# Kernel optimization log

Hardware: AMD Instinct MI355X
Metric: run time of the kernel (lower is better)

The kernel has to match this reference:

```python
import jax, jax.numpy as jnp
import numpy as np

SCALE = 1.0 / np.float32(64.0 ** 0.5)  # module hard-codes sqrt(64), not sqrt(d)


def setup_inputs() -> dict:
    key = jax.random.key(0)
    k1, k2 = jax.random.split(key)
    x = jax.random.normal(k1, (8, 2048, 1024), dtype=jnp.float32)
    kernel = jax.random.normal(k2, (3, 1024, 1024), dtype=jnp.float32) * 0.02
    return {"x": x, "kernel": kernel}


def reference(x, kernel):
    # x: [B, S, D], kernel: [3, D, O]
    wq = jnp.einsum('bsd,do->bso', x, kernel[0])
    wk = jnp.einsum('bsd,do->bso', x, kernel[1])
    wv = jnp.einsum('bsd,do->bso', x, kernel[2])
    scores = jnp.einsum('bqo,bko->bqk', wq, wk) * SCALE  # [B, S, S]
    attn = jax.nn.softmax(scores, axis=-1)
    return jnp.einsum('bqk,bko->bqo', attn, wv)  # [B, S, O]
```

## Files before the change

### kernel.cpp

```cpp
#include <hip/hip_runtime.h>

typedef _Float16 f16;
typedef f16 f16x8 __attribute__((ext_vector_type(8)));
typedef f16 f16x4 __attribute__((ext_vector_type(4)));
typedef float f32x4 __attribute__((ext_vector_type(4)));

#define GLD_LDS16(g, l) __builtin_amdgcn_global_load_lds( \
    (const __attribute__((address_space(1))) void*)(g),   \
    (__attribute__((address_space(3))) void*)(l), 16, 0, 0)

__device__ __forceinline__ void bar() {
    asm volatile("" ::: "memory");
    __builtin_amdgcn_s_barrier();
    asm volatile("" ::: "memory");
}
#define WAIT_VM(n) { asm volatile("s_waitcnt vmcnt(" #n ")" ::: "memory"); \
                     __builtin_amdgcn_sched_barrier(0); }
#define LGKM(n)    { asm volatile("s_waitcnt lgkmcnt(" #n ")" ::: "memory"); \
                     __builtin_amdgcn_sched_barrier(0); }

__global__ __launch_bounds__(256) void cast_f32_f16(const float* __restrict__ x,
                                                    f16* __restrict__ xh) {
    long i = ((long)blockIdx.x * 256 + threadIdx.x) * 8;
    float4 a = *(const float4*)&x[i];
    float4 b = *(const float4*)&x[i + 4];
    f16x8 v;
    v[0] = (f16)a.x; v[1] = (f16)a.y; v[2] = (f16)a.z; v[3] = (f16)a.w;
    v[4] = (f16)b.x; v[5] = (f16)b.y; v[6] = (f16)b.z; v[7] = (f16)b.w;
    *(f16x8*)&xh[i] = v;
}

__global__ __launch_bounds__(256) void cast_transpose_1k(const float* __restrict__ Wi,
                                                         f16* __restrict__ WTi) {
    __shared__ float tile[64][65];
    const int d0 = blockIdx.y * 64;
    const int o0 = blockIdx.x * 64;
    const int t = threadIdx.x;
#pragma unroll
    for (int j = 0; j < 4; ++j) {
        int idx = t + j * 256;
        int r = idx >> 4;
        int c4 = (idx & 15) * 4;
        float4 v = *(const float4*)&Wi[(long)(d0 + r) * 1024 + o0 + c4];
        tile[r][c4 + 0] = v.x; tile[r][c4 + 1] = v.y;
        tile[r][c4 + 2] = v.z; tile[r][c4 + 3] = v.w;
    }
    __syncthreads();
#pragma unroll
    for (int j = 0; j < 2; ++j) {
        int idx = t + j * 256;
        int ol = idx >> 3;
        int c8 = (idx & 7) * 8;
        f16x8 v;
#pragma unroll
        for (int e = 0; e < 8; ++e) v[e] = (f16)tile[c8 + e][ol];
        *(f16x8*)&WTi[(long)(o0 + ol) * 1024 + d0 + c8] = v;
    }
}

template <int MODE>
__global__ __launch_bounds__(512, 2)
void gemm256(const f16* __restrict__ A, const f16* __restrict__ B,
             void* __restrict__ Cv, const float* __restrict__ dinv,
             float* __restrict__ psum,
             int lda, int ldb, int K,
             long sA, long sB, long sC, int ldc, float scale) {
    extern __shared__ __align__(16) char smem[];
    const int tid = threadIdx.x;
    const int lane = tid & 63;
    const int wave = tid >> 6;
    const int wm = wave >> 2;
    const int wn = wave & 3;
    const int z = blockIdx.z;

    const int o_ = blockIdx.x + gridDim.x * blockIdx.y;
    const int nwg = gridDim.x * gridDim.y;
    const int sw = (o_ & 7) * (nwg >> 3) + (o_ >> 3);
    const int bx = sw % gridDim.x;
    const int by = sw / gridDim.x;

    const long m_base = (long)by * 256;
    const long n_base = (long)bx * 256;
    const f16* Ab = A + (long)z * sA;
    const f16* Bb = B + (long)z * sB;

    const int c_r0 = tid >> 3;
    const int c_col = ((tid & 7) * 8) ^ ((c_r0 & 7) << 3);
    const long oA0 = (m_base + c_r0) * (long)lda + c_col;
    const long oA1 = oA0 + 64L * lda;
    const long oB0 = (n_base + c_r0) * (long)ldb + c_col;
    const long oB1 = oB0 + 64L * ldb;

#define ST_A0(bf_, kt_) { long k0_ = (long)(kt_) * 64; \
    char* d_ = smem + (bf_) * 65536 + tid * 16; \
    GLD_LDS16(Ab + oA0 + k0_, d_); GLD_LDS16(Ab + oA1 + k0_, d_ + 8192); }
#define ST_A1(bf_, kt_) { long k0_ = (long)(kt_) * 64 + 128L * lda; \
    char* d_ = smem + (bf_) * 65536 + 16384 + tid * 16; \
    GLD_LDS16(Ab + oA0 + k0_, d_); GLD_LDS16(Ab + oA1 + k0_, d_ + 8192); }
#define ST_B0(bf_, kt_) { long k0_ = (long)(kt_) * 64; \
    char* d_ = smem + (bf_) * 65536 + 32768 + tid * 16; \
    GLD_LDS16(Bb + oB0 + k0_, d_); GLD_LDS16(Bb + oB1 + k0_, d_ + 8192); }
#define ST_B1(bf_, kt_) { long k0_ = (long)(kt_) * 64 + 128L * ldb; \
    char* d_ = smem + (bf_) * 65536 + 49152 + tid * 16; \
    GLD_LDS16(Bb + oB0 + k0_, d_); GLD_LDS16(Bb + oB1 + k0_, d_ + 8192); }

    const int fr = lane & 15;
    const int rq = lane >> 4;
    const int cs0 = (rq * 16) ^ ((lane & 7) << 4);
    const int cs1 = cs0 ^ 64;
    const int aoff = wm * 16384 + fr * 128;
    const int boff = 32768 + (wn >> 1) * 16384 + (wn & 1) * 8192 + fr * 128;

    f32x4 acc[8][4];
#pragma unroll
    for (int i = 0; i < 8; ++i)
#pragma unroll
        for (int j = 0; j < 4; ++j) acc[i][j] = (f32x4){0.f, 0.f, 0.f, 0.f};

    const int NT = K >> 6;

    ST_B0(0, 0); ST_B1(0, 0); ST_A0(0, 0); ST_A1(0, 0);
    WAIT_VM(4);
    ST_B0(1, 1); ST_B1(1, 1); ST_A0(1, 1);
    WAIT_VM(6);
    bar();

    for (int j = 0; j < NT; ++j) {
        char* bufb = smem + (j & 1) * 65536;
        const char* Ap = bufb + aoff;
        const char* Bp = bufb + boff;
        f16x8 af[4][2], bf[4][2];

#pragma unroll
        for (int i = 0; i < 4; ++i) {
            af[i][0] = *(const f16x8*)(Ap + i * 2048 + cs0);
            af[i][1] = *(const f16x8*)(Ap + i * 2048 + cs1);
        }
        __builtin_amdgcn_sched_barrier(0);
#pragma unroll
        for (int ni = 0; ni < 2; ++ni) {
            bf[ni][0] = *(const f16x8*)(Bp + ni * 2048 + cs0);
            bf[ni][1] = *(const f16x8*)(Bp + ni * 2048 + cs1);
        }
        __builtin_amdgcn_sched_barrier(0);
#pragma unroll
        for (int ni = 2; ni < 4; ++ni) {
            bf[ni][0] = *(const f16x8*)(Bp + ni * 2048 + cs0);
            bf[ni][1] = *(const f16x8*)(Bp + ni * 2048 + cs1);
        }
        if (j + 1 < NT) ST_A1((j + 1) & 1, j + 1);
        bar();
        LGKM(4);
        __builtin_amdgcn_s_setprio(1);
#pragma unroll
        for (int ks = 0; ks < 2; ++ks)
#pragma unroll
            for (int i = 0; i < 4; ++i)
#pragma unroll
                for (int n = 0; n < 2; ++n)
                    acc[i][n] = __builtin_amdgcn_mfma_f32_16x16x32_f16(
                        af[i][ks], bf[n][ks], acc[i][n], 0, 0, 0);
        __builtin_amdgcn_s_setprio(0);
        bar();

        LGKM(0);
        if (j + 2 < NT) ST_B0(j & 1, j + 2);
        bar();
        __builtin_amdgcn_s_setprio(1);
#pragma unroll
        for (int ks = 0; ks < 2; ++ks)
#pragma unroll
            for (int i = 0; i < 4; ++i)
#pragma unroll
                for (int n = 0; n < 2; ++n)
                    acc[i][2 + n] = __builtin_amdgcn_mfma_f32_16x16x32_f16(
                        af[i][ks], bf[2 + n][ks], acc[i][2 + n], 0, 0, 0);
        __builtin_amdgcn_s_setprio(0);
        bar();

#pragma unroll
        for (int i = 0; i < 4; ++i) {
            af[i][0] = *(const f16x8*)(Ap + (4 + i) * 2048 + cs0);
            af[i][1] = *(const f16x8*)(Ap + (4 + i) * 2048 + cs1);
        }
        if (j + 2 < NT) ST_B1(j & 1, j + 2);
        bar();
        LGKM(0);
        __builtin_amdgcn_s_setprio(1);
#pragma unroll
        for (int ks = 0; ks < 2; ++ks)
#pragma unroll
            for (int i = 0; i < 4; ++i)
#pragma unroll
                for (int n = 0; n < 2; ++n)
                    acc[4 + i][n] = __builtin_amdgcn_mfma_f32_16x16x32_f16(
                        af[i][ks], bf[n][ks], acc[4 + i][n], 0, 0, 0);
        __builtin_amdgcn_s_setprio(0);
        bar();

        if (j + 2 < NT) {
            ST_A0(j & 1, j + 2);
            WAIT_VM(6);
        } else if (j + 1 < NT) {
            WAIT_VM(0);
        }
        bar();
        __builtin_amdgcn_s_setprio(1);
#pragma unroll
        for (int ks = 0; ks < 2; ++ks)
#pragma unroll
            for (int i = 0; i < 4; ++i)
#pragma unroll
                for (int n = 0; n < 2; ++n)
                    acc[4 + i][2 + n] = __builtin_amdgcn_mfma_f32_16x16x32_f16(
                        af[i][ks], bf[2 + n][ks], acc[4 + i][2 + n], 0, 0, 0);
        __builtin_amdgcn_s_setprio(0);
        bar();
    }

    if constexpr (MODE == 0) {
        f16* C = (f16*)Cv + (long)z * sC;
        float p[8][4];
#pragma unroll
        for (int mi = 0; mi < 8; ++mi)
#pragma unroll
            for (int jj = 0; jj < 4; ++jj) p[mi][jj] = 0.f;
#pragma unroll
        for (int mi = 0; mi < 8; ++mi) {
            long r0 = m_base + wm * 128 + mi * 16 + rq * 4;
#pragma unroll
            for (int ni = 0; ni < 4; ++ni) {
                long c = n_base + wn * 64 + ni * 16 + fr;
#pragma unroll
                for (int jj = 0; jj < 4; ++jj) {
                    float e = __expf(acc[mi][ni][jj] * scale - 4.0f);
                    C[(r0 + jj) * (long)ldc + c] = (f16)e;
                    p[mi][jj] += e;
                }
            }
        }
#pragma unroll
        for (int mi = 0; mi < 8; ++mi)
#pragma unroll
            for (int jj = 0; jj < 4; ++jj)
#pragma unroll
                for (int o = 8; o; o >>= 1)
                    p[mi][jj] += __shfl_xor(p[mi][jj], o);
        float* wsum = (float*)smem;
        if (fr == 0) {
#pragma unroll
            for (int mi = 0; mi < 8; ++mi)
#pragma unroll
                for (int jj = 0; jj < 4; ++jj)
                    wsum[wn * 256 + wm * 128 + mi * 16 + rq * 4 + jj] = p[mi][jj];
        }
        bar();
        if (tid < 256) {
            float s = wsum[tid] + wsum[256 + tid] + wsum[512 + tid] + wsum[768 + tid];
            psum[((long)z * 2048 + m_base + tid) * 8 + bx] = s;
        }
    } else {
#pragma unroll
        for (int mi = 0; mi < 8; ++mi) {
            long r0 = m_base + wm * 128 + mi * 16 + rq * 4;
#pragma unroll
            for (int ni = 0; ni < 4; ++ni) {
                long c = n_base + wn * 64 + ni * 16 + fr;
                if constexpr (MODE == 1) {
                    f16* C = (f16*)Cv + (long)z * sC;
#pragma unroll
                    for (int jj = 0; jj < 4; ++jj)
                        C[(r0 + jj) * (long)ldc + c] = (f16)(acc[mi][ni][jj] * scale);
                } else if constexpr (MODE == 2) {
                    float* C = (float*)Cv + (long)z * sC;
#pragma unroll
                    for (int jj = 0; jj < 4; ++jj)
                        C[(r0 + jj) * (long)ldc + c] =
                            acc[mi][ni][jj] * dinv[(long)z * 2048 + r0 + jj];
                } else {
                    if (c < 1024) {
                        f16* T = (f16*)Cv;
#pragma unroll
                        for (int jj = 0; jj < 4; ++jj)
                            T[(r0 + jj) * 1024L + c] = (f16)acc[mi][ni][jj];
                    } else {
                        f16* VT = (f16*)((char*)Cv + 67108864);
                        long o = c - 1024;
                        long b = r0 >> 11;
                        long s = r0 & 2047;
                        f16x4 v;
#pragma unroll
                        for (int jj = 0; jj < 4; ++jj) v[jj] = (f16)acc[mi][ni][jj];
                        *(f16x4*)&VT[b * 2097152L + o * 2048L + s] = v;
                    }
                }
            }
        }
    }
#undef ST_A0
#undef ST_A1
#undef ST_B0
#undef ST_B1
}

__global__ __launch_bounds__(256) void reduce_dinv(const float* __restrict__ psum,
                                                   float* __restrict__ dinv) {
    int r = blockIdx.x * 256 + threadIdx.x;
    float4 a = *(const float4*)&psum[(long)r * 8];
    float4 b = *(const float4*)&psum[(long)r * 8 + 4];
    dinv[r] = 1.f / (a.x + a.y + a.z + a.w + b.x + b.y + b.z + b.w);
}

extern "C" void kernel_launch(void* const* d_in, const int* in_sizes, int n_in,
                              void* d_out, int out_size, void* d_ws, size_t ws_size,
                              hipStream_t stream) {
    const float* x = (const float*)d_in[0];
    const float* w = (const float*)d_in[1];
    float* out = (float*)d_out;
    char* ws = (char*)d_ws;

    f16* th  = (f16*)(ws + 0);
    f16* xh  = (f16*)(ws + 33554432);
    f16* vt  = (f16*)(ws + 67108864);
    char* spB = ws + 100663296;
    f16* whq = (f16*)(spB);
    f16* whk = (f16*)(spB + 2097152);
    f16* bTV = (f16*)(spB + 4194304);
    f16* sp  = (f16*)(spB);
    float* dinv = (float*)(ws + 0);
    float* psum = (float*)d_out;

    cast_f32_f16<<<1024, 256, 0, stream>>>(w, whq);
    cast_transpose_1k<<<dim3(16, 16), 256, 0, stream>>>(w + 2097152, bTV + 1048576);
    cast_f32_f16<<<8192, 256, 0, stream>>>(x, xh);

    gemm256<1><<<dim3(4, 4, 1), 512, 131072, stream>>>(
        whk, whq, bTV, nullptr, nullptr, 1024, 1024, 1024, 0L, 0L, 0L, 1024, 1.0f);

    gemm256<4><<<dim3(8, 64, 1), 512, 131072, stream>>>(
        xh, bTV, ws, nullptr, nullptr, 1024, 1024, 1024, 0L, 0L, 0L, 0, 1.0f);

    gemm256<0><<<dim3(8, 8, 8), 512, 131072, stream>>>(
        th, xh, sp, nullptr, psum, 1024, 1024, 1024,
        2097152L, 2097152L, 4194304L, 2048, 0.125f);

    reduce_dinv<<<64, 256, 0, stream>>>(psum, dinv);

    gemm256<2><<<dim3(4, 8, 8), 512, 131072, stream>>>(
        sp, vt, out, dinv, nullptr, 2048, 2048, 2048,
        4194304L, 2097152L, 2097152L, 1024, 1.0f);
}
```

Baseline: 295.6 us.

## Make GEMM workgroups loop over multiple N tiles and add small-tile weight GEMM

The main GEMM kernel gains a TILES parameter so each workgroup computes two consecutive 256-wide N tiles. It prefetches the next tile's first K stages while writing out the current epilogue, which halves the grid for the projection and score GEMMs. The tiny weight-product GEMM (whk·whqᵀ) moves to a new 128x128-tile kernel, gemm_mp, so it launches 64 workgroups instead of 16. The row-sum partials are now written per wave without an LDS reduction, so psum grows to 32 entries per row and reduce_dinv sums 32 values. The risk is fewer workgroups per launch (lower occupancy and worse tail balance) and more scattered psum writes.

```diff
diff --git a/kernel.cpp b/kernel.cpp
--- a/kernel.cpp
+++ b/kernel.cpp
@@ -58,7 +58,77 @@
     }
 }
 
-template <int MODE>
+__global__ __launch_bounds__(256, 2)
+void gemm_mp(const f16* __restrict__ A, const f16* __restrict__ B,
+             f16* __restrict__ C) {
+    __shared__ f16x8 ls[2][2][4][128];
+    const int tid = threadIdx.x;
+    const int lane = tid & 63;
+    const int wave = tid >> 6;
+    const int wm = wave >> 1;
+    const int wn = wave & 1;
+    const long m_base = (long)blockIdx.y * 128;
+    const long n_base = (long)blockIdx.x * 128;
+
+    const int i1 = tid + 256;
+    const int kb0 = tid >> 7, r0 = tid & 127;
+    const int kb1 = i1 >> 7, r1 = i1 & 127;
+    const f16* gA0 = A + (m_base + r0) * 1024L + kb0 * 8;
+    const f16* gA1 = A + (m_base + r1) * 1024L + kb1 * 8;
+    const f16* gB0 = B + (n_base + r0) * 1024L + kb0 * 8;
+    const f16* gB1 = B + (n_base + r1) * 1024L + kb1 * 8;
+
+    auto stage = [&](int buf, int k0) {
+        GLD_LDS16(gA0 + k0, &ls[buf][0][kb0][r0]);
+        GLD_LDS16(gA1 + k0, &ls[buf][0][kb1][r1]);
+        GLD_LDS16(gB0 + k0, &ls[buf][1][kb0][r0]);
+        GLD_LDS16(gB1 + k0, &ls[buf][1][kb1][r1]);
+    };
+
+    f32x4 acc[4][4];
+#pragma unroll
+    for (int i = 0; i < 4; ++i)
+#pragma unroll
+        for (int j = 0; j < 4; ++j) acc[i][j] = (f32x4){0.f, 0.f, 0.f, 0.f};
+
+    stage(0, 0);
+    WAIT_VM(0);
+    bar();
+    int cur = 0;
+    const int kb = lane >> 4;
+    const int fr = lane & 15;
+    for (int t = 0; t < 32; ++t) {
+        if (t + 1 < 32) stage(cur ^ 1, (t + 1) << 5);
+        f16x8 af[4], bf[4];
+#pragma unroll
+        for (int mi = 0; mi < 4; ++mi) af[mi] = ls[cur][0][kb][wm * 64 + mi * 16 + fr];
+#pragma unroll
+        for (int ni = 0; ni < 4; ++ni) bf[ni] = ls[cur][1][kb][wn * 64 + ni * 16 + fr];
+#pragma unroll
+        for (int mi = 0; mi < 4; ++mi)
+#pragma unroll
+            for (int ni = 0; ni < 4; ++ni)
+                acc[mi][ni] = __builtin_amdgcn_mfma_f32_16x16x32_f16(
+                    af[mi], bf[ni], acc[mi][ni], 0, 0, 0);
+        WAIT_VM(0);
+        bar();
+        cur ^= 1;
+    }
+    const int rq = lane >> 4;
+#pragma unroll
+    for (int mi = 0; mi < 4; ++mi) {
+        long r0_ = m_base + wm * 64 + mi * 16 + rq * 4;
+#pragma unroll
+        for (int ni = 0; ni < 4; ++ni) {
+            long c = n_base + wn * 64 + ni * 16 + fr;
+#pragma unroll
+            for (int j = 0; j < 4; ++j)
+                C[(r0_ + j) * 1024L + c] = (f16)acc[mi][ni][j];
+        }
+    }
+}
+
+template <int MODE, int TILES>
 __global__ __launch_bounds__(512, 2)
 void gemm256(const f16* __restrict__ A, const f16* __restrict__ B,
              void* __restrict__ Cv, const float* __restrict__ dinv,
@@ -76,11 +146,10 @@
     const int o_ = blockIdx.x + gridDim.x * blockIdx.y;
     const int nwg = gridDim.x * gridDim.y;
     const int sw = (o_ & 7) * (nwg >> 3) + (o_ >> 3);
-    const int bx = sw % gridDim.x;
+    const int bxb = sw % gridDim.x;
     const int by = sw / gridDim.x;
 
     const long m_base = (long)by * 256;
-    const long n_base = (long)bx * 256;
     const f16* Ab = A + (long)z * sA;
     const f16* Bb = B + (long)z * sB;
 
@@ -88,8 +157,8 @@
     const int c_col = ((tid & 7) * 8) ^ ((c_r0 & 7) << 3);
     const long oA0 = (m_base + c_r0) * (long)lda + c_col;
     const long oA1 = oA0 + 64L * lda;
-    const long oB0 = (n_base + c_r0) * (long)ldb + c_col;
-    const long oB1 = oB0 + 64L * ldb;
+    long oB0 = ((long)(bxb * TILES) * 256 + c_r0) * (long)ldb + c_col;
+    long oB1 = oB0 + 64L * ldb;
 
 #define ST_A0(bf_, kt_) { long k0_ = (long)(kt_) * 64; \
     char* d_ = smem + (bf_) * 65536 + tid * 16; \
@@ -111,12 +180,6 @@
     const int aoff = wm * 16384 + fr * 128;
     const int boff = 32768 + (wn >> 1) * 16384 + (wn & 1) * 8192 + fr * 128;
 
-    f32x4 acc[8][4];
-#pragma unroll
-    for (int i = 0; i < 8; ++i)
-#pragma unroll
-        for (int j = 0; j < 4; ++j) acc[i][j] = (f32x4){0.f, 0.f, 0.f, 0.f};
-
     const int NT = K >> 6;
 
     ST_B0(0, 0); ST_B1(0, 0); ST_A0(0, 0); ST_A1(0, 0);
@@ -125,176 +188,191 @@
     WAIT_VM(6);
     bar();
 
-    for (int j = 0; j < NT; ++j) {
-        char* bufb = smem + (j & 1) * 65536;
-        const char* Ap = bufb + aoff;
-        const char* Bp = bufb + boff;
-        f16x8 af[4][2], bf[4][2];
-
-#pragma unroll
-        for (int i = 0; i < 4; ++i) {
-            af[i][0] = *(const f16x8*)(Ap + i * 2048 + cs0);
-            af[i][1] = *(const f16x8*)(Ap + i * 2048 + cs1);
+    for (int tt = 0; tt < TILES; ++tt) {
+        const long n_base = (long)(bxb * TILES + tt) * 256;
+
+        f32x4 acc[8][4];
+#pragma unroll
+        for (int i = 0; i < 8; ++i)
+#pragma unroll
+            for (int j = 0; j < 4; ++j) acc[i][j] = (f32x4){0.f, 0.f, 0.f, 0.f};
+
+        for (int j = 0; j < NT; ++j) {
+            char* bufb = smem + (j & 1) * 65536;
+            const char* Ap = bufb + aoff;
+            const char* Bp = bufb + boff;
+            f16x8 af[4][2], bf[4][2];
+
+#pragma unroll
+            for (int i = 0; i < 4; ++i) {
+                af[i][0] = *(const f16x8*)(Ap + i * 2048 + cs0);
+                af[i][1] = *(const f16x8*)(Ap + i * 2048 + cs1);
+            }
+            __builtin_amdgcn_sched_barrier(0);
+#pragma unroll
+            for (int ni = 0; ni < 2; ++ni) {
+                bf[ni][0] = *(const f16x8*)(Bp + ni * 2048 + cs0);
+                bf[ni][1] = *(const f16x8*)(Bp + ni * 2048 + cs1);
+            }
+            __builtin_amdgcn_sched_barrier(0);
+#pragma unroll
+            for (int ni = 2; ni < 4; ++ni) {
+                bf[ni][0] = *(const f16x8*)(Bp + ni * 2048 + cs0);
+                bf[ni][1] = *(const f16x8*)(Bp + ni * 2048 + cs1);
+            }
+            if (j + 1 < NT) ST_A1((j + 1) & 1, j + 1);
+            bar();
+            LGKM(4);
+            __builtin_amdgcn_s_setprio(1);
+#pragma unroll
+            for (int ks = 0; ks < 2; ++ks)
+#pragma unroll
+                for (int i = 0; i < 4; ++i)
+#pragma unroll
+                    for (int n = 0; n < 2; ++n)
+                        acc[i][n] = __builtin_amdgcn_mfma_f32_16x16x32_f16(
+                            af[i][ks], bf[n][ks], acc[i][n], 0, 0, 0);
+            __builtin_amdgcn_s_setprio(0);
+            bar();
+
+            LGKM(0);
+            if (j + 2 < NT) ST_B0(j & 1, j + 2);
+            bar();
+            __builtin_amdgcn_s_setprio(1);
+#pragma unroll
+            for (int ks = 0; ks < 2; ++ks)
+#pragma unroll
+                for (int i = 0; i < 4; ++i)
+#pragma unroll
+                    for (int n = 0; n < 2; ++n)
+                        acc[i][2 + n] = __builtin_amdgcn_mfma_f32_16x16x32_f16(
+                            af[i][ks], bf[2 + n][ks], acc[i][2 + n], 0, 0, 0);
+            __builtin_amdgcn_s_setprio(0);
+            bar();
+
+#pragma unroll
+            for (int i = 0; i < 4; ++i) {
+                af[i][0] = *(const f16x8*)(Ap + (4 + i) * 2048 + cs0);
+                af[i][1] = *(const f16x8*)(Ap + (4 + i) * 2048 + cs1);
+            }
+            if (j + 2 < NT) ST_B1(j & 1, j + 2);
+            bar();
+            LGKM(0);
+            __builtin_amdgcn_s_setprio(1);
+#pragma unroll
+            for (int ks = 0; ks < 2; ++ks)
+#pragma unroll
+                for (int i = 0; i < 4; ++i)
+#pragma unroll
+                    for (int n = 0; n < 2; ++n)
+                        acc[4 + i][n] = __builtin_amdgcn_mfma_f32_16x16x32_f16(
+                            af[i][ks], bf[n][ks], acc[4 + i][n], 0, 0, 0);
+            __builtin_amdgcn_s_setprio(0);
+            bar();
+
+            if (j + 2 < NT) {
+                ST_A0(j & 1, j + 2);
+                WAIT_VM(6);
+            } else if (j + 1 < NT) {
+                WAIT_VM(0);
+            }
+            bar();
+            __builtin_amdgcn_s_setprio(1);
+#pragma unroll
+            for (int ks = 0; ks < 2; ++ks)
+#pragma unroll
+                for (int i = 0; i < 4; ++i)
+#pragma unroll
+                    for (int n = 0; n < 2; ++n)
+                        acc[4 + i][2 + n] = __builtin_amdgcn_mfma_f32_16x16x32_f16(
+                            af[i][ks], bf[2 + n][ks], acc[4 + i][2 + n], 0, 0, 0);
+            __builtin_amdgcn_s_setprio(0);
+            bar();
         }
-        __builtin_amdgcn_sched_barrier(0);
-#pragma unroll
-        for (int ni = 0; ni < 2; ++ni) {
-            bf[ni][0] = *(const f16x8*)(Bp + ni * 2048 + cs0);
-            bf[ni][1] = *(const f16x8*)(Bp + ni * 2048 + cs1);
+
+        if (tt + 1 < TILES) {
+            oB0 = ((long)(bxb * TILES + tt + 1) * 256 + c_r0) * (long)ldb + c_col;
+            oB1 = oB0 + 64L * ldb;
+            ST_B0(0, 0); ST_B1(0, 0); ST_A0(0, 0); ST_A1(0, 0);
+            ST_B0(1, 1); ST_B1(1, 1); ST_A0(1, 1);
         }
-        __builtin_amdgcn_sched_barrier(0);
-#pragma unroll
-        for (int ni = 2; ni < 4; ++ni) {
-            bf[ni][0] = *(const f16x8*)(Bp + ni * 2048 + cs0);
-            bf[ni][1] = *(const f16x8*)(Bp + ni * 2048 + cs1);
-        }
-        if (j + 1 < NT) ST_A1((j + 1) & 1, j + 1);
-        bar();
-        LGKM(4);
-        __builtin_amdgcn_s_setprio(1);
-#pragma unroll
-        for (int ks = 0; ks < 2; ++ks)
-#pragma unroll
-            for (int i = 0; i < 4; ++i)
-#pragma unroll
-                for (int n = 0; n < 2; ++n)
-                    acc[i][n] = __builtin_amdgcn_mfma_f32_16x16x32_f16(
-                        af[i][ks], bf[n][ks], acc[i][n], 0, 0, 0);
-        __builtin_amdgcn_s_setprio(0);
-        bar();
-
-        LGKM(0);
-        if (j + 2 < NT) ST_B0(j & 1, j + 2);
-        bar();
-        __builtin_amdgcn_s_setprio(1);
-#pragma unroll
-        for (int ks = 0; ks < 2; ++ks)
-#pragma unroll
-            for (int i = 0; i < 4; ++i)
-#pragma unroll
-                for (int n = 0; n < 2; ++n)
-                    acc[i][2 + n] = __builtin_amdgcn_mfma_f32_16x16x32_f16(
-                        af[i][ks], bf[2 + n][ks], acc[i][2 + n], 0, 0, 0);
-        __builtin_amdgcn_s_setprio(0);
-        bar();
-
-#pragma unroll
-        for (int i = 0; i < 4; ++i) {
-            af[i][0] = *(const f16x8*)(Ap + (4 + i) * 2048 + cs0);
-            af[i][1] = *(const f16x8*)(Ap + (4 + i) * 2048 + cs1);
-        }
-        if (j + 2 < NT) ST_B1(j & 1, j + 2);
-        bar();
-        LGKM(0);
-        __builtin_amdgcn_s_setprio(1);
-#pragma unroll
-        for (int ks = 0; ks < 2; ++ks)
-#pragma unroll
-            for (int i = 0; i < 4; ++i)
-#pragma unroll
-                for (int n = 0; n < 2; ++n)
-                    acc[4 + i][n] = __builtin_amdgcn_mfma_f32_16x16x32_f16(
-                        af[i][ks], bf[n][ks], acc[4 + i][n], 0, 0, 0);
-        __builtin_amdgcn_s_setprio(0);
-        bar();
-
-        if (j + 2 < NT) {
-            ST_A0(j & 1, j + 2);
-            WAIT_VM(6);
-        } else if (j + 1 < NT) {
-            WAIT_VM(0);
-        }
-        bar();
-        __builtin_amdgcn_s_setprio(1);
-#pragma unroll
-        for (int ks = 0; ks < 2; ++ks)
-#pragma unroll
-            for (int i = 0; i < 4; ++i)
-#pragma unroll
-                for (int n = 0; n < 2; ++n)
-                    acc[4 + i][2 + n] = __builtin_amdgcn_mfma_f32_16x16x32_f16(
-                        af[i][ks], bf[2 + n][ks], acc[4 + i][2 + n], 0, 0, 0);
-        __builtin_amdgcn_s_setprio(0);
-        bar();
-    }
-
-    if constexpr (MODE == 0) {
-        f16* C = (f16*)Cv + (long)z * sC;
-        float p[8][4];
-#pragma unroll
-        for (int mi = 0; mi < 8; ++mi)
-#pragma unroll
-            for (int jj = 0; jj < 4; ++jj) p[mi][jj] = 0.f;
-#pragma unroll
-        for (int mi = 0; mi < 8; ++mi) {
-            long r0 = m_base + wm * 128 + mi * 16 + rq * 4;
-#pragma unroll
-            for (int ni = 0; ni < 4; ++ni) {
-                long c = n_base + wn * 64 + ni * 16 + fr;
-#pragma unroll
-                for (int jj = 0; jj < 4; ++jj) {
-                    float e = __expf(acc[mi][ni][jj] * scale - 4.0f);
-                    C[(r0 + jj) * (long)ldc + c] = (f16)e;
-                    p[mi][jj] += e;
-                }
-            }
-        }
-#pragma unroll
-        for (int mi = 0; mi < 8; ++mi)
-#pragma unroll
-            for (int jj = 0; jj < 4; ++jj)
-#pragma unroll
-                for (int o = 8; o; o >>= 1)
-                    p[mi][jj] += __shfl_xor(p[mi][jj], o);
-        float* wsum = (float*)smem;
-        if (fr == 0) {
+
+        if constexpr (MODE == 0) {
+            f16* C = (f16*)Cv + (long)z * sC;
+            float p[8][4];
 #pragma unroll
             for (int mi = 0; mi < 8; ++mi)
 #pragma unroll
-                for (int jj = 0; jj < 4; ++jj)
-                    wsum[wn * 256 + wm * 128 + mi * 16 + rq * 4 + jj] = p[mi][jj];
-        }
-        bar();
-        if (tid < 256) {
-            float s = wsum[tid] + wsum[256 + tid] + wsum[512 + tid] + wsum[768 + tid];
-            psum[((long)z * 2048 + m_base + tid) * 8 + bx] = s;
-        }
-    } else {
-#pragma unroll
-        for (int mi = 0; mi < 8; ++mi) {
-            long r0 = m_base + wm * 128 + mi * 16 + rq * 4;
-#pragma unroll
-            for (int ni = 0; ni < 4; ++ni) {
-                long c = n_base + wn * 64 + ni * 16 + fr;
-                if constexpr (MODE == 1) {
-                    f16* C = (f16*)Cv + (long)z * sC;
-#pragma unroll
-                    for (int jj = 0; jj < 4; ++jj)
-                        C[(r0 + jj) * (long)ldc + c] = (f16)(acc[mi][ni][jj] * scale);
-                } else if constexpr (MODE == 2) {
-                    float* C = (float*)Cv + (long)z * sC;
-#pragma unroll
-                    for (int jj = 0; jj < 4; ++jj)
-                        C[(r0 + jj) * (long)ldc + c] =
-                            acc[mi][ni][jj] * dinv[(long)z * 2048 + r0 + jj];
-                } else {
-                    if (c < 1024) {
-                        f16* T = (f16*)Cv;
-#pragma unroll
-                        for (int jj = 0; jj < 4; ++jj)
-                            T[(r0 + jj) * 1024L + c] = (f16)acc[mi][ni][jj];
-                    } else {
-                        f16* VT = (f16*)((char*)Cv + 67108864);
-                        long o = c - 1024;
-                        long b = r0 >> 11;
-                        long s = r0 & 2047;
-                        f16x4 v;
-#pragma unroll
-                        for (int jj = 0; jj < 4; ++jj) v[jj] = (f16)acc[mi][ni][jj];
-                        *(f16x4*)&VT[b * 2097152L + o * 2048L + s] = v;
+                for (int jj = 0; jj < 4; ++jj) p[mi][jj] = 0.f;
+#pragma unroll
+            for (int mi = 0; mi < 8; ++mi) {
+                long r0 = m_base + wm * 128 + mi * 16 + rq * 4;
+#pragma unroll
+                for (int ni = 0; ni < 4; ++ni) {
+                    long c = n_base + wn * 64 + ni * 16 + fr;
+#pragma unroll
+                    for (int jj = 0; jj < 4; ++jj) {
+                        float e = __expf(acc[mi][ni][jj] * scale - 4.0f);
+                        C[(r0 + jj) * (long)ldc + c] = (f16)e;
+                        p[mi][jj] += e;
                     }
                 }
             }
+#pragma unroll
+            for (int mi = 0; mi < 8; ++mi)
+#pragma unroll
+                for (int jj = 0; jj < 4; ++jj)
+#pragma unroll
+                    for (int o = 8; o; o >>= 1)
+                        p[mi][jj] += __shfl_xor(p[mi][jj], o);
+            if (fr == 0) {
+                const int bx_n = (int)(n_base >> 8);
+#pragma unroll
+                for (int mi = 0; mi < 8; ++mi) {
+                    long r0 = m_base + wm * 128 + mi * 16 + rq * 4;
+#pragma unroll
+                    for (int jj = 0; jj < 4; ++jj)
+                        psum[((long)z * 2048 + r0 + jj) * 32 + bx_n * 4 + wn] =
+                            p[mi][jj];
+                }
+            }
+        } else {
+#pragma unroll
+            for (int mi = 0; mi < 8; ++mi) {
+                long r0 = m_base + wm * 128 + mi * 16 + rq * 4;
+#pragma unroll
+                for (int ni = 0; ni < 4; ++ni) {
+                    long c = n_base + wn * 64 + ni * 16 + fr;
+                    if constexpr (MODE == 2) {
+                        float* C = (float*)Cv + (long)z * sC;
+#pragma unroll
+                        for (int jj = 0; jj < 4; ++jj)
+                            C[(r0 + jj) * (long)ldc + c] =
+                                acc[mi][ni][jj] * dinv[(long)z * 2048 + r0 + jj];
+                    } else {
+                        if (c < 1024) {
+                            f16* T = (f16*)Cv;
+#pragma unroll
+                            for (int jj = 0; jj < 4; ++jj)
+                                T[(r0 + jj) * 1024L + c] = (f16)acc[mi][ni][jj];
+                        } else {
+                            f16* VT = (f16*)((char*)Cv + 67108864);
+                            long o = c - 1024;
+                            long b = r0 >> 11;
+                            long s = r0 & 2047;
+                            f16x4 v;
+#pragma unroll
+                            for (int jj = 0; jj < 4; ++jj) v[jj] = (f16)acc[mi][ni][jj];
+                            *(f16x4*)&VT[b * 2097152L + o * 2048L + s] = v;
+                        }
+                    }
+                }
+            }
+        }
+
+        if (tt + 1 < TILES) {
+            WAIT_VM(6);
+            bar();
         }
     }
 #undef ST_A0
@@ -306,9 +384,13 @@
 __global__ __launch_bounds__(256) void reduce_dinv(const float* __restrict__ psum,
                                                    float* __restrict__ dinv) {
     int r = blockIdx.x * 256 + threadIdx.x;
-    float4 a = *(const float4*)&psum[(long)r * 8];
-    float4 b = *(const float4*)&psum[(long)r * 8 + 4];
-    dinv[r] = 1.f / (a.x + a.y + a.z + a.w + b.x + b.y + b.z + b.w);
+    float s = 0.f;
+#pragma unroll
+    for (int k = 0; k < 8; ++k) {
+        float4 a = *(const float4*)&psum[(long)r * 32 + k * 4];
+        s += a.x + a.y + a.z + a.w;
+    }
+    dinv[r] = 1.f / s;
 }
 
 extern "C" void kernel_launch(void* const* d_in, const int* in_sizes, int n_in,
@@ -334,19 +416,18 @@
     cast_transpose_1k<<<dim3(16, 16), 256, 0, stream>>>(w + 2097152, bTV + 1048576);
     cast_f32_f16<<<8192, 256, 0, stream>>>(x, xh);
 
-    gemm256<1><<<dim3(4, 4, 1), 512, 131072, stream>>>(
-        whk, whq, bTV, nullptr, nullptr, 1024, 1024, 1024, 0L, 0L, 0L, 1024, 1.0f);
-
-    gemm256<4><<<dim3(8, 64, 1), 512, 131072, stream>>>(
+    gemm_mp<<<dim3(8, 8), 256, 0, stream>>>(whk, whq, bTV);
+
+    gemm256<4, 2><<<dim3(4, 64, 1), 512, 131072, stream>>>(
         xh, bTV, ws, nullptr, nullptr, 1024, 1024, 1024, 0L, 0L, 0L, 0, 1.0f);
 
-    gemm256<0><<<dim3(8, 8, 8), 512, 131072, stream>>>(
+    gemm256<0, 2><<<dim3(4, 8, 8), 512, 131072, stream>>>(
         th, xh, sp, nullptr, psum, 1024, 1024, 1024,
         2097152L, 2097152L, 4194304L, 2048, 0.125f);
 
     reduce_dinv<<<64, 256, 0, stream>>>(psum, dinv);
 
-    gemm256<2><<<dim3(4, 8, 8), 512, 131072, stream>>>(
+    gemm256<2, 1><<<dim3(4, 8, 8), 512, 131072, stream>>>(
         sp, vt, out, dinv, nullptr, 2048, 2048, 2048,
         4194304L, 2097152L, 2097152L, 1024, 1.0f);
 }
```

New measurement: 307.0 us. 1.04x slower.
